# Kernel tuning notes

Measured on AMD Instinct MI355X. Metric: run time of the kernel, lower is better.

The kernel has to match this reference:

```python
import jax, jax.numpy as jnp
import numpy as np

N, C = 8192, 256
CQK = C // 8  # q/k projection dim = 32


def setup_inputs() -> dict:
    key = jax.random.key(0)
    k1, k2, k3, k4, k5 = jax.random.split(key, 5)
    f = jax.random.normal(k1, (N, C), dtype=jnp.float32)
    Wqk = jax.random.normal(k2, (CQK, C), dtype=jnp.float32) * (1.0 / np.sqrt(C))
    Wv = jax.random.normal(k3, (C, C), dtype=jnp.float32) * (1.0 / np.sqrt(C))
    bv = jax.random.normal(k4, (C,), dtype=jnp.float32) * 0.01
    gamma = jax.random.normal(k5, (1,), dtype=jnp.float32)
    return {"f": f, "Wqk": Wqk, "Wv": Wv, "bv": bv, "gamma": gamma}


def reference(f, Wqk, Wv, bv, gamma):
    # f: [N, C] point features. 1x1 convs over the point dim == per-point linear.
    q = f @ Wqk.T                      # [N, CQK] (q and k share weights)
    # energy[i, j] = <q_i, k_j>; q == k here, no 1/sqrt(d) scaling (faithful)
    energy = q @ q.T                   # [N, N]
    attn = jax.nn.softmax(energy, axis=-1)  # softmax over last dim (dim=-1)
    v = f @ Wv.T + bv                  # [N, C]
    # torch: bmm(x_v [1,C,N], attn [1,N,N]) -> out[c, j] = sum_i v[i, c] * attn[i, j]
    attn_out = jnp.einsum('ij,ic->jc', attn, v)  # [N, C]
    return gamma[0] * attn_out + f     # [N, C]
```

## Files before the change

kernel.cpp:

```cpp
#include <hip/hip_runtime.h>
#include <hip/hip_bf16.h>

#define NN 8192
#define CC 256
#define CQK 32
#define JS 4

using bf16x8 = __attribute__((ext_vector_type(8))) short;
using f16x8  = __attribute__((ext_vector_type(8))) _Float16;
using s16x4  = __attribute__((ext_vector_type(4))) short;
using f32x4  = __attribute__((ext_vector_type(4))) float;
using f32x16 = __attribute__((ext_vector_type(16))) float;

static __device__ __forceinline__ unsigned short f2bf(float x) {
    union { __hip_bfloat16 h; unsigned short u; } cv;
    cv.h = __float2bfloat16(x);
    return cv.u;
}
static __device__ __forceinline__ float bf2f(unsigned short u) {
    union { unsigned u; float f; } cv;
    cv.u = (unsigned)u << 16;
    return cv.f;
}
static __device__ __forceinline__ float fexp2(float x) { return __builtin_amdgcn_exp2f(x); }
static __device__ __forceinline__ int packbf(float lo, float hi) {
    union { float f; unsigned u; } a, b;
    a.f = lo; b.f = hi;
    return (int)((b.u & 0xFFFF0000u) | (a.u >> 16));
}

__global__ __launch_bounds__(256) void proj_kernel(
    const float* __restrict__ f, const float* __restrict__ Wqk,
    const float* __restrict__ Wv, const float* __restrict__ bv,
    unsigned short* __restrict__ qf, unsigned short* __restrict__ vB)
{
    __shared__ __align__(16) float fl[8][CC];
    const int t = threadIdx.x;

    if (blockIdx.x < 1024) {
        const int r0 = blockIdx.x * 8;
        {
            const float4* src = (const float4*)(f + (size_t)r0 * CC);
            float4* dst = (float4*)&fl[0][0];
            dst[t]       = src[t];
            dst[t + 256] = src[t + 256];
        }
        __syncthreads();
        const int cq = t & 31;
        const int rg = t >> 5;
        const float4* w4 = (const float4*)(Wqk + (size_t)cq * CC);
        float a = 0.f;
        for (int k4 = 0; k4 < 64; ++k4) {
            float4 wq = w4[k4];
            const float4 fv = *(const float4*)&fl[rg][k4 * 4];
            a = fmaf(wq.x, fv.x, a);
            a = fmaf(wq.y, fv.y, a);
            a = fmaf(wq.z, fv.z, a);
            a = fmaf(wq.w, fv.w, a);
        }
        a *= 1.2011224087864498f;
        union { _Float16 h; unsigned short u; } cv;
        cv.h = (_Float16)a;
        qf[(size_t)(r0 + rg) * CQK + cq] = cv.u;
    } else {
        const int lane = t & 63;
        const int w    = t >> 6;
        const int l31  = lane & 31;
        const int h    = lane >> 5;
        const int nb   = (blockIdx.x - 1024) * 32;
        const int cb   = w * 64;

        f32x16 acc[2];
#pragma unroll
        for (int cf = 0; cf < 2; ++cf)
#pragma unroll
            for (int r = 0; r < 16; ++r) acc[cf][r] = 0.f;

        const float* frow = f + (size_t)(nb + l31) * CC;
#pragma unroll
        for (int ks = 0; ks < 16; ++ks) {
            const int k0 = ks * 16 + 8 * h;
            float4 a0 = *(const float4*)(frow + k0);
            float4 a1 = *(const float4*)(frow + k0 + 4);
            bf16x8 af;
            af[0] = (short)f2bf(a0.x); af[1] = (short)f2bf(a0.y);
            af[2] = (short)f2bf(a0.z); af[3] = (short)f2bf(a0.w);
            af[4] = (short)f2bf(a1.x); af[5] = (short)f2bf(a1.y);
            af[6] = (short)f2bf(a1.z); af[7] = (short)f2bf(a1.w);
#pragma unroll
            for (int cf = 0; cf < 2; ++cf) {
                const float* wrow = Wv + (size_t)(cb + 32 * cf + l31) * CC + k0;
                float4 b0 = *(const float4*)(wrow);
                float4 b1 = *(const float4*)(wrow + 4);
                bf16x8 bw;
                bw[0] = (short)f2bf(b0.x); bw[1] = (short)f2bf(b0.y);
                bw[2] = (short)f2bf(b0.z); bw[3] = (short)f2bf(b0.w);
                bw[4] = (short)f2bf(b1.x); bw[5] = (short)f2bf(b1.y);
                bw[6] = (short)f2bf(b1.z); bw[7] = (short)f2bf(b1.w);
                acc[cf] = __builtin_amdgcn_mfma_f32_32x32x16_bf16(af, bw, acc[cf], 0, 0, 0);
            }
        }
#pragma unroll
        for (int cf = 0; cf < 2; ++cf) {
            const int cg = cb + 32 * cf + l31;
            const float bvc = bv[cg];
#pragma unroll
            for (int rg = 0; rg < 4; ++rg) {
                const int ib = (nb >> 3) + rg;
                s16x4 pk;
#pragma unroll
                for (int r = 0; r < 4; ++r)
                    pk[r] = (short)f2bf(acc[cf][4 * rg + r] + bvc);
                *(s16x4*)(vB + ((size_t)ib * CC + cg) * 8 + 4 * h) = pk;
            }
        }
    }
}

__global__ __launch_bounds__(256, 4) void pass1_kernel(
    const unsigned short* __restrict__ qf,
    float* __restrict__ ps)
{
    const int t    = threadIdx.x;
    const int lane = t & 63;
    const int w    = t >> 6;
    const int l31  = lane & 31;
    const int h    = lane >> 5;
    const int i0   = (blockIdx.x & 255) * 32;
    const int js   = blockIdx.x >> 8;
    const int JCH  = NN / JS / 4;
    const int jbase = js * (NN / JS) + w * JCH;

    const size_t qir = (size_t)(i0 + l31) * CQK;
    const f16x8 bi0 = *(const f16x8*)(qf + qir + 8 * h);
    const f16x8 bi1 = *(const f16x8*)(qf + qir + 16 + 8 * h);

    float s = 0.f;

#pragma unroll 2
    for (int st = 0; st < JCH; st += 32) {
        const size_t qjr = (size_t)(jbase + st + l31) * CQK;
        const f16x8 aj0 = *(const f16x8*)(qf + qjr + 8 * h);
        const f16x8 aj1 = *(const f16x8*)(qf + qjr + 16 + 8 * h);
        f32x16 ee = {0,0,0,0,0,0,0,0,0,0,0,0,0,0,0,0};
        ee = __builtin_amdgcn_mfma_f32_32x32x16_f16(aj0, bi0, ee, 0, 0, 0);
        ee = __builtin_amdgcn_mfma_f32_32x32x16_f16(aj1, bi1, ee, 0, 0, 0);
        float a_ = 0.f;
#pragma unroll
        for (int r = 0; r < 16; ++r) a_ += fexp2(ee[r]);
        s += a_;
    }
    s += __shfl_xor(s, 32);

    __shared__ float rs[4][32];
    if (lane < 32) rs[w][l31] = s;
    __syncthreads();
    if (t < 32) {
        float sf = rs[0][t] + rs[1][t] + rs[2][t] + rs[3][t];
        ps[(size_t)js * NN + i0 + t] = sf;
    }
}

__global__ __launch_bounds__(256) void finalize_kernel(
    const float* __restrict__ ps, float* __restrict__ bias)
{
    int i = blockIdx.x * 256 + threadIdx.x;
    float s = ps[i];
#pragma unroll
    for (int k = 1; k < JS; ++k) s += ps[(size_t)k * NN + i];
    bias[i] = __builtin_amdgcn_logf(s);
}

#define LOADQF(A0, A1, NI)                                                     \
    {                                                                          \
        const size_t qnr = (size_t)((NI) + l31) * CQK;                         \
        A0 = *(const f16x8*)(qf + qnr + 8 * h);                                \
        A1 = *(const f16x8*)(qf + qnr + 16 + 8 * h);                           \
    }

#define LOADVF2(VF, I)                                                         \
    _Pragma("unroll")                                                          \
    for (int s2 = 0; s2 < 2; ++s2)                                             \
        _Pragma("unroll")                                                      \
        for (int cf = 0; cf < 4; ++cf)                                         \
            VF[s2][cf] = *(const bf16x8*)(                                     \
                vB + ((size_t)(((I) >> 3) + 2 * s2 + h) * CC + cb + 32 * cf + l31) * 8);

#define LOADB42(B4, I)                                                         \
    _Pragma("unroll")                                                          \
    for (int rg = 0; rg < 4; ++rg)                                             \
        B4[rg] = *(const f32x4*)(bias + (I) + 8 * rg + 4 * h);

#define ECOMPF(EE, A0, A1)                                                     \
    {                                                                          \
        f32x16 z_ = {0,0,0,0,0,0,0,0,0,0,0,0,0,0,0,0};                         \
        z_ = __builtin_amdgcn_mfma_f32_32x32x16_f16(A1, bj1, z_, 0, 0, 0);     \
        EE = __builtin_amdgcn_mfma_f32_32x32x16_f16(A0, bj0, z_, 0, 0, 0);     \
    }

#define FINISH2(EE, B4, VF)                                                    \
    {                                                                          \
        int d0[4], d1[4];                                                      \
        _Pragma("unroll")                                                      \
        for (int rg = 0; rg < 4; ++rg) {                                       \
            float p0 = fexp2(EE[4 * rg + 0] - B4[rg][0]);                      \
            float p1 = fexp2(EE[4 * rg + 1] - B4[rg][1]);                      \
            float p2 = fexp2(EE[4 * rg + 2] - B4[rg][2]);                      \
            float p3 = fexp2(EE[4 * rg + 3] - B4[rg][3]);                      \
            d0[rg] = packbf(p0, p1);                                           \
            d1[rg] = packbf(p2, p3);                                           \
        }                                                                      \
        _Pragma("unroll")                                                      \
        for (int s2 = 0; s2 < 2; ++s2) {                                       \
            const int a_ = d0[2 * s2], b_ = d0[2 * s2 + 1];                    \
            const int c_ = d1[2 * s2], d_ = d1[2 * s2 + 1];                    \
            const int pa = __shfl_xor(a_, 32);                                 \
            const int pb = __shfl_xor(b_, 32);                                 \
            const int pc = __shfl_xor(c_, 32);                                 \
            const int pd = __shfl_xor(d_, 32);                                 \
            union { int i[4]; bf16x8 v; } pf;                                  \
            pf.i[0] = h ? pb : a_;                                             \
            pf.i[1] = h ? pd : c_;                                             \
            pf.i[2] = h ? b_ : pa;                                             \
            pf.i[3] = h ? d_ : pc;                                             \
            _Pragma("unroll")                                                  \
            for (int cf = 0; cf < 4; ++cf)                                     \
                acc[cf] = __builtin_amdgcn_mfma_f32_32x32x16_bf16(             \
                    pf.v, VF[s2][cf], acc[cf], 0, 0, 0);                       \
        }                                                                      \
    }

template<int ISPLIT, bool DIRECT>
__global__ __launch_bounds__(256, 2) void pass2_kernel(
    const unsigned short* __restrict__ qf,
    const unsigned short* __restrict__ vB,
    const float* __restrict__ bias,
    const float* __restrict__ f,
    const float* __restrict__ gp,
    void* __restrict__ dstv)
{
    const int t    = threadIdx.x;
    const int lane = t & 63;
    const int w    = t >> 6;
    const int l31  = lane & 31;
    const int h    = lane >> 5;

    int jblk, isp;
    if (ISPLIT == 4) {
        const int bid = blockIdx.x;
        isp  = (bid & 7) >> 1;
        jblk = ((bid >> 3) << 1) | (bid & 1);
    } else if (ISPLIT == 2) {
        isp  = blockIdx.x & 1;
        jblk = blockIdx.x >> 1;
    } else {
        isp  = 0;
        jblk = blockIdx.x;
    }
    const int jb   = jblk * 64;
    const int jrow = jb + 32 * (w & 1);
    const int cb   = 128 * (w >> 1);
    const int IL   = NN / ISPLIT;
    const int ibase = isp * IL;
    const int iend  = ibase + IL;

    const size_t qjr = (size_t)(jrow + l31) * CQK;
    const f16x8 bj0 = *(const f16x8*)(qf + qjr + 8 * h);
    const f16x8 bj1 = *(const f16x8*)(qf + qjr + 16 + 8 * h);

    f32x16 acc[4];
#pragma unroll
    for (int cf = 0; cf < 4; ++cf)
#pragma unroll
        for (int r = 0; r < 16; ++r) acc[cf][r] = 0.f;

    f32x16 eeA, eeB;
    f32x4  b4A[4], b4B[4];
    f16x8  qa0, qa1, qb0, qb1;
    bf16x8 vfA[2][4], vfB[2][4];

    LOADQF(qa0, qa1, ibase)
    LOADB42(b4A, ibase)
    LOADVF2(vfA, ibase)
    ECOMPF(eeA, qa0, qa1)
    LOADQF(qb0, qb1, ibase + 32)
    LOADB42(b4B, ibase + 32)

    for (int i0s = ibase; i0s < iend; i0s += 64) {
        const int n1 = (i0s + 64 < iend) ? i0s + 64 : ibase;
        const int n2 = (i0s + 96 < iend) ? i0s + 96 : ibase;
        LOADVF2(vfB, i0s + 32)
        ECOMPF(eeB, qb0, qb1)
        LOADQF(qa0, qa1, n1)
        FINISH2(eeA, b4A, vfA)
        LOADB42(b4A, n1)
        LOADVF2(vfA, n1)
        ECOMPF(eeA, qa0, qa1)
        LOADQF(qb0, qb1, n2)
        FINISH2(eeB, b4B, vfB)
        LOADB42(b4B, n2)
    }

    if (DIRECT) {
        float* dst = (float*)dstv;
        const float g = gp[0];
#pragma unroll
        for (int cf = 0; cf < 4; ++cf) {
            const int c = cb + 32 * cf + l31;
#pragma unroll
            for (int rg = 0; rg < 4; ++rg)
#pragma unroll
                for (int r = 0; r < 4; ++r) {
                    const int j = jrow + 4 * h + r + 8 * rg;
                    dst[(size_t)j * CC + c] =
                        fmaf(g, acc[cf][4 * rg + r], f[(size_t)j * CC + c]);
                }
        }
    } else {
        unsigned short* part = (unsigned short*)dstv + (size_t)isp * NN * CC;
#pragma unroll
        for (int cf = 0; cf < 4; ++cf) {
            const int c = cb + 32 * cf + l31;
#pragma unroll
            for (int rg = 0; rg < 4; ++rg)
#pragma unroll
                for (int r = 0; r < 4; ++r) {
                    const int j = jrow + 4 * h + r + 8 * rg;
                    part[(size_t)j * CC + c] = f2bf(acc[cf][4 * rg + r]);
                }
        }
    }
}

template<int SPLIT>
__global__ __launch_bounds__(256) void reduce_kernel(
    const unsigned short* __restrict__ part, const float* __restrict__ f,
    const float* __restrict__ gp, float* __restrict__ out)
{
    size_t idx = (size_t)blockIdx.x * 256 + threadIdx.x;
    float s0 = 0.f, s1 = 0.f, s2 = 0.f, s3 = 0.f;
#pragma unroll
    for (int k = 0; k < SPLIT; ++k) {
        const s16x4 v = *(const s16x4*)(part + (size_t)k * NN * CC + idx * 4);
        s0 += bf2f((unsigned short)v[0]);
        s1 += bf2f((unsigned short)v[1]);
        s2 += bf2f((unsigned short)v[2]);
        s3 += bf2f((unsigned short)v[3]);
    }
    const f32x4 fv = ((const f32x4*)f)[idx];
    const float g = gp[0];
    f32x4 o;
    o[0] = fmaf(g, s0, fv[0]);
    o[1] = fmaf(g, s1, fv[1]);
    o[2] = fmaf(g, s2, fv[2]);
    o[3] = fmaf(g, s3, fv[3]);
    ((f32x4*)out)[idx] = o;
}

extern "C" void kernel_launch(void* const* d_in, const int* in_sizes, int n_in,
                              void* d_out, int out_size, void* d_ws, size_t ws_size,
                              hipStream_t stream) {
    const float* f     = (const float*)d_in[0];
    const float* Wqk   = (const float*)d_in[1];
    const float* Wv    = (const float*)d_in[2];
    const float* bv    = (const float*)d_in[3];
    const float* gamma = (const float*)d_in[4];
    float* out = (float*)d_out;

    char* ws = (char*)d_ws;
    unsigned short* qf  = (unsigned short*)ws;
    unsigned short* vB  = (unsigned short*)(ws + (1 << 20));
    float* ps   = (float*)(ws + (5 << 20));
    float* bias = (float*)(ws + (5 << 20) + (256 << 10));
    unsigned short* part = (unsigned short*)(ws + (6 << 20));

    proj_kernel<<<dim3(1024 + NN / 32), dim3(256), 0, stream>>>(f, Wqk, Wv, bv, qf, vB);
    pass1_kernel<<<dim3((NN / 32) * JS), dim3(256), 0, stream>>>(qf, ps);
    finalize_kernel<<<dim3(NN / 256), dim3(256), 0, stream>>>(ps, bias);

    const size_t PB = (size_t)NN * CC * 2;
    const size_t B0 = (size_t)6 << 20;
    if (ws_size >= B0 + 4 * PB) {
        pass2_kernel<4, false><<<dim3(128 * 4), dim3(256), 0, stream>>>(qf, vB, bias, f, gamma, part);
        reduce_kernel<4><<<dim3(NN * CC / 1024), dim3(256), 0, stream>>>(part, f, gamma, out);
    } else if (ws_size >= B0 + 2 * PB) {
        pass2_kernel<2, false><<<dim3(128 * 2), dim3(256), 0, stream>>>(qf, vB, bias, f, gamma, part);
        reduce_kernel<2><<<dim3(NN * CC / 1024), dim3(256), 0, stream>>>(part, f, gamma, out);
    } else {
        pass2_kernel<1, true><<<dim3(128), dim3(256), 0, stream>>>(qf, vB, bias, f, gamma, out);
    }
}
```

Before: 133.7 us.

## Move V projection into pass1 launch and stagger pass2 i-start per block

The V projection MFMA work moves out of the projection kernel into the pass1 launch as extra blocks, so it runs alongside the row-sum exp pass. The q projection becomes its own small kernel. Pass2 now starts its i-loop at a 32-row offset for alternating blocks and wraps modulo the i-range, so co-resident blocks read different qf/vB rows instead of hitting the same ones together. This adds some index arithmetic and bigger, mixed-workload pass1 blocks that may hurt occupancy balance.

```diff
diff --git a/kernel.cpp b/kernel.cpp
--- a/kernel.cpp
+++ b/kernel.cpp
@@ -29,46 +29,87 @@
     return (int)((b.u & 0xFFFF0000u) | (a.u >> 16));
 }
 
-__global__ __launch_bounds__(256) void proj_kernel(
+__global__ __launch_bounds__(256) void proj_q_kernel(
     const float* __restrict__ f, const float* __restrict__ Wqk,
-    const float* __restrict__ Wv, const float* __restrict__ bv,
-    unsigned short* __restrict__ qf, unsigned short* __restrict__ vB)
+    unsigned short* __restrict__ qf)
 {
     __shared__ __align__(16) float fl[8][CC];
-    const int t = threadIdx.x;
-
-    if (blockIdx.x < 1024) {
-        const int r0 = blockIdx.x * 8;
-        {
-            const float4* src = (const float4*)(f + (size_t)r0 * CC);
-            float4* dst = (float4*)&fl[0][0];
-            dst[t]       = src[t];
-            dst[t + 256] = src[t + 256];
-        }
+    const int t  = threadIdx.x;
+    const int r0 = blockIdx.x * 8;
+    {
+        const float4* src = (const float4*)(f + (size_t)r0 * CC);
+        float4* dst = (float4*)&fl[0][0];
+        dst[t]       = src[t];
+        dst[t + 256] = src[t + 256];
+    }
+    __syncthreads();
+    const int cq = t & 31;
+    const int rg = t >> 5;
+    const float4* w4 = (const float4*)(Wqk + (size_t)cq * CC);
+    float a = 0.f;
+    for (int k4 = 0; k4 < 64; ++k4) {
+        float4 wq = w4[k4];
+        const float4 fv = *(const float4*)&fl[rg][k4 * 4];
+        a = fmaf(wq.x, fv.x, a);
+        a = fmaf(wq.y, fv.y, a);
+        a = fmaf(wq.z, fv.z, a);
+        a = fmaf(wq.w, fv.w, a);
+    }
+    a *= 1.2011224087864498f;
+    union { _Float16 h; unsigned short u; } cv;
+    cv.h = (_Float16)a;
+    qf[(size_t)(r0 + rg) * CQK + cq] = cv.u;
+}
+
+__global__ __launch_bounds__(256, 4) void pass1v_kernel(
+    const unsigned short* __restrict__ qf,
+    const float* __restrict__ f, const float* __restrict__ Wv,
+    const float* __restrict__ bv,
+    float* __restrict__ ps, unsigned short* __restrict__ vB)
+{
+    __shared__ float rs[4][32];
+    const int t    = threadIdx.x;
+    const int lane = t & 63;
+    const int w    = t >> 6;
+    const int l31  = lane & 31;
+    const int h    = lane >> 5;
+
+    if (blockIdx.x < (NN / 32) * JS) {
+        const int i0   = (blockIdx.x & 255) * 32;
+        const int js   = blockIdx.x >> 8;
+        const int JCH  = NN / JS / 4;
+        const int jbase = js * (NN / JS) + w * JCH;
+
+        const size_t qir = (size_t)(i0 + l31) * CQK;
+        const f16x8 bi0 = *(const f16x8*)(qf + qir + 8 * h);
+        const f16x8 bi1 = *(const f16x8*)(qf + qir + 16 + 8 * h);
+
+        float s = 0.f;
+
+#pragma unroll 2
+        for (int st = 0; st < JCH; st += 32) {
+            const size_t qjr = (size_t)(jbase + st + l31) * CQK;
+            const f16x8 aj0 = *(const f16x8*)(qf + qjr + 8 * h);
+            const f16x8 aj1 = *(const f16x8*)(qf + qjr + 16 + 8 * h);
+            f32x16 ee = {0,0,0,0,0,0,0,0,0,0,0,0,0,0,0,0};
+            ee = __builtin_amdgcn_mfma_f32_32x32x16_f16(aj0, bi0, ee, 0, 0, 0);
+            ee = __builtin_amdgcn_mfma_f32_32x32x16_f16(aj1, bi1, ee, 0, 0, 0);
+            float a_ = 0.f;
+#pragma unroll
+            for (int r = 0; r < 16; ++r) a_ += fexp2(ee[r]);
+            s += a_;
+        }
+        s += __shfl_xor(s, 32);
+
+        if (lane < 32) rs[w][l31] = s;
         __syncthreads();
-        const int cq = t & 31;
-        const int rg = t >> 5;
-        const float4* w4 = (const float4*)(Wqk + (size_t)cq * CC);
-        float a = 0.f;
-        for (int k4 = 0; k4 < 64; ++k4) {
-            float4 wq = w4[k4];
-            const float4 fv = *(const float4*)&fl[rg][k4 * 4];
-            a = fmaf(wq.x, fv.x, a);
-            a = fmaf(wq.y, fv.y, a);
-            a = fmaf(wq.z, fv.z, a);
-            a = fmaf(wq.w, fv.w, a);
-        }
-        a *= 1.2011224087864498f;
-        union { _Float16 h; unsigned short u; } cv;
-        cv.h = (_Float16)a;
-        qf[(size_t)(r0 + rg) * CQK + cq] = cv.u;
+        if (t < 32) {
+            float sf = rs[0][t] + rs[1][t] + rs[2][t] + rs[3][t];
+            ps[(size_t)js * NN + i0 + t] = sf;
+        }
     } else {
-        const int lane = t & 63;
-        const int w    = t >> 6;
-        const int l31  = lane & 31;
-        const int h    = lane >> 5;
-        const int nb   = (blockIdx.x - 1024) * 32;
-        const int cb   = w * 64;
+        const int nb = (blockIdx.x - (NN / 32) * JS) * 32;
+        const int cb = w * 64;
 
         f32x16 acc[2];
 #pragma unroll
@@ -114,50 +155,6 @@
                 *(s16x4*)(vB + ((size_t)ib * CC + cg) * 8 + 4 * h) = pk;
             }
         }
-    }
-}
-
-__global__ __launch_bounds__(256, 4) void pass1_kernel(
-    const unsigned short* __restrict__ qf,
-    float* __restrict__ ps)
-{
-    const int t    = threadIdx.x;
-    const int lane = t & 63;
-    const int w    = t >> 6;
-    const int l31  = lane & 31;
-    const int h    = lane >> 5;
-    const int i0   = (blockIdx.x & 255) * 32;
-    const int js   = blockIdx.x >> 8;
-    const int JCH  = NN / JS / 4;
-    const int jbase = js * (NN / JS) + w * JCH;
-
-    const size_t qir = (size_t)(i0 + l31) * CQK;
-    const f16x8 bi0 = *(const f16x8*)(qf + qir + 8 * h);
-    const f16x8 bi1 = *(const f16x8*)(qf + qir + 16 + 8 * h);
-
-    float s = 0.f;
-
-#pragma unroll 2
-    for (int st = 0; st < JCH; st += 32) {
-        const size_t qjr = (size_t)(jbase + st + l31) * CQK;
-        const f16x8 aj0 = *(const f16x8*)(qf + qjr + 8 * h);
-        const f16x8 aj1 = *(const f16x8*)(qf + qjr + 16 + 8 * h);
-        f32x16 ee = {0,0,0,0,0,0,0,0,0,0,0,0,0,0,0,0};
-        ee = __builtin_amdgcn_mfma_f32_32x32x16_f16(aj0, bi0, ee, 0, 0, 0);
-        ee = __builtin_amdgcn_mfma_f32_32x32x16_f16(aj1, bi1, ee, 0, 0, 0);
-        float a_ = 0.f;
-#pragma unroll
-        for (int r = 0; r < 16; ++r) a_ += fexp2(ee[r]);
-        s += a_;
-    }
-    s += __shfl_xor(s, 32);
-
-    __shared__ float rs[4][32];
-    if (lane < 32) rs[w][l31] = s;
-    __syncthreads();
-    if (t < 32) {
-        float sf = rs[0][t] + rs[1][t] + rs[2][t] + rs[3][t];
-        ps[(size_t)js * NN + i0 + t] = sf;
     }
 }
 
@@ -244,25 +241,25 @@
     const int w    = t >> 6;
     const int l31  = lane & 31;
     const int h    = lane >> 5;
+    const int bid  = blockIdx.x;
 
     int jblk, isp;
     if (ISPLIT == 4) {
-        const int bid = blockIdx.x;
         isp  = (bid & 7) >> 1;
         jblk = ((bid >> 3) << 1) | (bid & 1);
     } else if (ISPLIT == 2) {
-        isp  = blockIdx.x & 1;
-        jblk = blockIdx.x >> 1;
+        isp  = bid & 1;
+        jblk = bid >> 1;
     } else {
         isp  = 0;
-        jblk = blockIdx.x;
+        jblk = bid;
     }
     const int jb   = jblk * 64;
     const int jrow = jb + 32 * (w & 1);
     const int cb   = 128 * (w >> 1);
     const int IL   = NN / ISPLIT;
     const int ibase = isp * IL;
-    const int iend  = ibase + IL;
+    const int off  = ((bid ^ (bid >> 8)) & 1) * 32;
 
     const size_t qjr = (size_t)(jrow + l31) * CQK;
     const f16x8 bj0 = *(const f16x8*)(qf + qjr + 8 * h);
@@ -279,17 +276,22 @@
     f16x8  qa0, qa1, qb0, qb1;
     bf16x8 vfA[2][4], vfB[2][4];
 
-    LOADQF(qa0, qa1, ibase)
-    LOADB42(b4A, ibase)
-    LOADVF2(vfA, ibase)
+    const int m = IL - 1;
+    const int iA0 = ibase + (off & m);
+    const int iB0 = ibase + ((off + 32) & m);
+
+    LOADQF(qa0, qa1, iA0)
+    LOADB42(b4A, iA0)
+    LOADVF2(vfA, iA0)
     ECOMPF(eeA, qa0, qa1)
-    LOADQF(qb0, qb1, ibase + 32)
-    LOADB42(b4B, ibase + 32)
-
-    for (int i0s = ibase; i0s < iend; i0s += 64) {
-        const int n1 = (i0s + 64 < iend) ? i0s + 64 : ibase;
-        const int n2 = (i0s + 96 < iend) ? i0s + 96 : ibase;
-        LOADVF2(vfB, i0s + 32)
+    LOADQF(qb0, qb1, iB0)
+    LOADB42(b4B, iB0)
+
+    for (int k = 0; k < IL; k += 64) {
+        const int iB = ibase + ((k + 32 + off) & m);
+        const int n1 = ibase + ((k + 64 + off) & m);
+        const int n2 = ibase + ((k + 96 + off) & m);
+        LOADVF2(vfB, iB)
         ECOMPF(eeB, qb0, qb1)
         LOADQF(qa0, qa1, n1)
         FINISH2(eeA, b4A, vfA)
@@ -374,8 +376,9 @@
     float* bias = (float*)(ws + (5 << 20) + (256 << 10));
     unsigned short* part = (unsigned short*)(ws + (6 << 20));
 
-    proj_kernel<<<dim3(1024 + NN / 32), dim3(256), 0, stream>>>(f, Wqk, Wv, bv, qf, vB);
-    pass1_kernel<<<dim3((NN / 32) * JS), dim3(256), 0, stream>>>(qf, ps);
+    proj_q_kernel<<<dim3(NN / 8), dim3(256), 0, stream>>>(f, Wqk, qf);
+    pass1v_kernel<<<dim3((NN / 32) * JS + NN / 32), dim3(256), 0, stream>>>(
+        qf, f, Wv, bv, ps, vB);
     finalize_kernel<<<dim3(NN / 256), dim3(256), 0, stream>>>(ps, bias);
 
     const size_t PB = (size_t)NN * CC * 2;
```

Measured after the change: 128.9 us. -3.6%, faster.
